# Kernel tuning notes

Hardware: AMD Instinct MI355X
Metric: run time of the kernel (lower is better)

Reference implementation:

```python
import jax, jax.numpy as jnp
import numpy as np

RAMP_SIZE = 8.0  # init arg ramp_size
EPS = 1e-8


def setup_inputs() -> dict:
    key = jax.random.key(0)
    k1, = jax.random.split(key, 1)
    max_size = 32
    mask_len = 8
    K = 2 * mask_len + 1
    x = jax.random.normal(k1, (8, 8, 64, 64, K * K), dtype=jnp.float32)
    current_val = 0.5 * jnp.ones((1, 1), dtype=jnp.float32)  # init_val=0.5
    mask_template = jnp.linspace(1.0 - max_size, 0.0, max_size, dtype=jnp.float32)
    return {"x": x, "current_val": current_val, "mask_template": mask_template,
            "mask_len": mask_len}


def _build_mask(current_val, mask_template, mask_len):
    max_size = mask_template.shape[0]
    # one_d_mask: (1, max_size) -> soft ramp in [0,1]
    one_d = (mask_template[None, :] + current_val * max_size) / RAMP_SIZE + 1.0
    one_d = jnp.clip(one_d, 0.0, 1.0)[:, -mask_len:]  # (1, mask_len)
    L = mask_len
    K = 2 * L + 1
    r = jnp.arange(K)
    # Chebyshev distance from center; ring at distance d was written with one_d[0, L-d]
    d = jnp.maximum(jnp.abs(r[:, None] - L), jnp.abs(r[None, :] - L))  # (K, K)
    idx = jnp.clip(L - d, 0, L - 1)
    mask2d = jnp.where(d == 0, jnp.ones((), one_d.dtype), one_d[0, idx])
    return mask2d.reshape(1, 1, 1, 1, K * K)


def reference(x, current_val, mask_template, mask_len):
    mask = _build_mask(current_val, mask_template, mask_len)
    x = x * mask
    return x / (jnp.sum(x, axis=-1, keepdims=True) + EPS)
```

## Files before the change

### kernel.cpp

```cpp
#include <hip/hip_runtime.h>


constexpr int L   = 8;
constexpr int K   = 2 * L + 1;
constexpr int KK  = K * K;
constexpr int NPL = (KK + 63) / 64;
constexpr int WAVES_PER_BLOCK = 4;

__global__ __launch_bounds__(256) void adamask_kernel(
    const float* __restrict__ x,
    const float* __restrict__ cur_val,
    const float* __restrict__ tmpl,
    float* __restrict__ out,
    int nrows, int max_size)
{
    const int lane = threadIdx.x & 63;
    const int wave = threadIdx.x >> 6;
    const long long row = (long long)blockIdx.x * WAVES_PER_BLOCK + wave;
    if (row >= nrows) return;

    const float cv = cur_val[0];

    float m[NPL];
#pragma unroll
    for (int k = 0; k < NPL; ++k) {
        const int idx = lane + 64 * k;
        float mv = 0.0f;
        if (idx < KK) {
            const int r = idx / K;
            const int c = idx - r * K;
            const int d = max(abs(r - L), abs(c - L));
            if (d == 0) {
                mv = 1.0f;
            } else {
                const int j = min(max(L - d, 0), L - 1);
                const float od =
                    (tmpl[max_size - L + j] + cv * (float)max_size) / 8.0f + 1.0f;
                mv = fminf(fmaxf(od, 0.0f), 1.0f);
            }
        }
        m[k] = mv;
    }

    const float* __restrict__ xr = x + row * KK;
    float* __restrict__ orow     = out + row * KK;

    float  v[NPL];
    double s = 0.0;
#pragma unroll
    for (int k = 0; k < NPL; ++k) {
        const int idx = lane + 64 * k;
        const float xv = (idx < KK) ? xr[idx] : 0.0f;
        v[k] = xv * m[k];
        s += (double)v[k];
    }

#pragma unroll
    for (int off = 32; off >= 1; off >>= 1)
        s += __shfl_xor(s, off, 64);

    const double inv = 1.0 / (s + 1e-8);

#pragma unroll
    for (int k = 0; k < NPL; ++k) {
        const int idx = lane + 64 * k;
        if (idx < KK) orow[idx] = (float)((double)v[k] * inv);
    }
}

extern "C" void kernel_launch(void* const* d_in, const int* in_sizes, int n_in,
                              void* d_out, int out_size, void* d_ws, size_t ws_size,
                              hipStream_t stream)
{
    const float* x    = (const float*)d_in[0];
    const float* cv   = (const float*)d_in[1];
    const float* tmpl = (const float*)d_in[2];
    float* out = (float*)d_out;

    const int nrows    = in_sizes[0] / KK;
    const int max_size = in_sizes[2];

    const int blocks = (nrows + WAVES_PER_BLOCK - 1) / WAVES_PER_BLOCK;
    adamask_kernel<<<blocks, 64 * WAVES_PER_BLOCK, 0, stream>>>(
        x, cv, tmpl, out, nrows, max_size);
}
```

Measured before the change: 494.0 us.

## Process four rows per wave with float4 vectorized loads and shared mask

Each wave now handles a group of four 289-element rows as one contiguous 1156-float span, so it can use aligned float4 loads and stores. The old layout left lanes idle on each row's odd-sized tail. The mask is computed once per block into shared memory instead of per lane in registers. Four separate double accumulators give per-row sums, at the cost of more index arithmetic and shuffles per element. The code assumes the row count is divisible by four.

```diff
diff --git a/kernel.cpp b/kernel.cpp
--- a/kernel.cpp
+++ b/kernel.cpp
@@ -4,67 +4,104 @@
 constexpr int L   = 8;
 constexpr int K   = 2 * L + 1;
 constexpr int KK  = K * K;
-constexpr int NPL = (KK + 63) / 64;
-constexpr int WAVES_PER_BLOCK = 4;
+constexpr int RPG = 4;
+constexpr int GF  = KK * RPG;
+constexpr int GF4 = GF / 4;
+constexpr int WPB = 4;
 
 __global__ __launch_bounds__(256) void adamask_kernel(
-    const float* __restrict__ x,
+    const float4* __restrict__ x,
     const float* __restrict__ cur_val,
     const float* __restrict__ tmpl,
-    float* __restrict__ out,
-    int nrows, int max_size)
+    float4* __restrict__ out,
+    int ngroups, int max_size)
 {
-    const int lane = threadIdx.x & 63;
-    const int wave = threadIdx.x >> 6;
-    const long long row = (long long)blockIdx.x * WAVES_PER_BLOCK + wave;
-    if (row >= nrows) return;
+    __shared__ float smask[KK];
 
-    const float cv = cur_val[0];
+    const int tid = threadIdx.x;
 
-    float m[NPL];
-#pragma unroll
-    for (int k = 0; k < NPL; ++k) {
-        const int idx = lane + 64 * k;
-        float mv = 0.0f;
-        if (idx < KK) {
-            const int r = idx / K;
-            const int c = idx - r * K;
+    {
+        const float cv = cur_val[0];
+        for (int i = tid; i < KK; i += 256) {
+            const int r = i / K;
+            const int c = i - r * K;
             const int d = max(abs(r - L), abs(c - L));
-            if (d == 0) {
-                mv = 1.0f;
-            } else {
+            float mv = 1.0f;
+            if (d != 0) {
                 const int j = min(max(L - d, 0), L - 1);
                 const float od =
-                    (tmpl[max_size - L + j] + cv * (float)max_size) / 8.0f + 1.0f;
+                    (tmpl[max_size - L + j] + cv * (float)max_size) * 0.125f + 1.0f;
                 mv = fminf(fmaxf(od, 0.0f), 1.0f);
             }
+            smask[i] = mv;
         }
-        m[k] = mv;
     }
+    __syncthreads();
 
-    const float* __restrict__ xr = x + row * KK;
-    float* __restrict__ orow     = out + row * KK;
+    const int lane = tid & 63;
+    const int wave = tid >> 6;
+    const long long grp = (long long)blockIdx.x * WPB + wave;
+    if (grp >= ngroups) return;
 
-    float  v[NPL];
-    double s = 0.0;
+    const float4* __restrict__ xg = x + grp * GF4;
+    float4* __restrict__ og       = out + grp * GF4;
+
+    float4 v[5];
+    double acc0 = 0.0, acc1 = 0.0, acc2 = 0.0, acc3 = 0.0;
+
 #pragma unroll
-    for (int k = 0; k < NPL; ++k) {
-        const int idx = lane + 64 * k;
-        const float xv = (idx < KK) ? xr[idx] : 0.0f;
-        v[k] = xv * m[k];
-        s += (double)v[k];
+    for (int k = 0; k < 5; ++k) {
+        const int i4 = lane + 64 * k;
+        if (i4 < GF4) {
+            float4 xv = xg[i4];
+            float e[4] = {xv.x, xv.y, xv.z, xv.w};
+            const int pbase = 4 * i4;
+#pragma unroll
+            for (int j = 0; j < 4; ++j) {
+                const int p = pbase + j;
+                const int r = (p >= KK) + (p >= 2 * KK) + (p >= 3 * KK);
+                const float val = e[j] * smask[p - r * KK];
+                e[j] = val;
+                const double dv = (double)val;
+                if (r == 0)      acc0 += dv;
+                else if (r == 1) acc1 += dv;
+                else if (r == 2) acc2 += dv;
+                else             acc3 += dv;
+            }
+            v[k] = make_float4(e[0], e[1], e[2], e[3]);
+        } else {
+            v[k] = make_float4(0.f, 0.f, 0.f, 0.f);
+        }
     }
 
 #pragma unroll
-    for (int off = 32; off >= 1; off >>= 1)
-        s += __shfl_xor(s, off, 64);
+    for (int off = 32; off >= 1; off >>= 1) {
+        acc0 += __shfl_xor(acc0, off, 64);
+        acc1 += __shfl_xor(acc1, off, 64);
+        acc2 += __shfl_xor(acc2, off, 64);
+        acc3 += __shfl_xor(acc3, off, 64);
+    }
 
-    const double inv = 1.0 / (s + 1e-8);
+    const float i0 = (float)(1.0 / (acc0 + 1e-8));
+    const float i1 = (float)(1.0 / (acc1 + 1e-8));
+    const float i2 = (float)(1.0 / (acc2 + 1e-8));
+    const float i3 = (float)(1.0 / (acc3 + 1e-8));
 
 #pragma unroll
-    for (int k = 0; k < NPL; ++k) {
-        const int idx = lane + 64 * k;
-        if (idx < KK) orow[idx] = (float)((double)v[k] * inv);
+    for (int k = 0; k < 5; ++k) {
+        const int i4 = lane + 64 * k;
+        if (i4 < GF4) {
+            float e[4] = {v[k].x, v[k].y, v[k].z, v[k].w};
+            const int pbase = 4 * i4;
+#pragma unroll
+            for (int j = 0; j < 4; ++j) {
+                const int p = pbase + j;
+                const int r = (p >= KK) + (p >= 2 * KK) + (p >= 3 * KK);
+                const float iv = (r == 0) ? i0 : (r == 1) ? i1 : (r == 2) ? i2 : i3;
+                e[j] *= iv;
+            }
+            og[i4] = make_float4(e[0], e[1], e[2], e[3]);
+        }
     }
 }
 
@@ -79,8 +116,9 @@
 
     const int nrows    = in_sizes[0] / KK;
     const int max_size = in_sizes[2];
+    const int ngroups  = nrows / RPG;
 
-    const int blocks = (nrows + WAVES_PER_BLOCK - 1) / WAVES_PER_BLOCK;
-    adamask_kernel<<<blocks, 64 * WAVES_PER_BLOCK, 0, stream>>>(
-        x, cv, tmpl, out, nrows, max_size);
+    const int blocks = (ngroups + WPB - 1) / WPB;
+    adamask_kernel<<<blocks, 64 * WPB, 0, stream>>>(
+        (const float4*)x, cv, tmpl, (float4*)out, ngroups, max_size);
 }
```

Result: no change. 488.7 us (-1.1%).
